# Performance work log

Hardware: AMD Instinct MI355X
Metric: run time of the kernel (lower is better)

Reference implementation:

```python
import jax, jax.numpy as jnp
import numpy as np

IMAGE_SIZE = 512
STRIDES = (8, 16, 32)
W_SEG, W_DET, W_CLS = 1.0, 1.0, 0.5


def _bce_logits(x, y):
    # numerically stable binary cross entropy with logits (broadcasts y)
    return jnp.maximum(x, 0.0) - x * y + jnp.log1p(jnp.exp(-jnp.abs(x)))


def _focal_loss_mean(logits, targets, num_classes, alpha=0.25, gamma=2.0):
    # sigmoid focal loss; targets are class indices, -1 (or any negative) => all-background row
    t = jax.nn.one_hot(targets, num_classes, dtype=logits.dtype)
    p = jax.nn.sigmoid(logits)
    ce = _bce_logits(logits, t)
    p_t = p * t + (1.0 - p) * (1.0 - t)
    a_t = alpha * t + (1.0 - alpha) * (1.0 - t)
    return jnp.mean(a_t * (1.0 - p_t) ** gamma * ce)


def _det_scale_loss(cls_logits, reg_preds, cent_preds, boxes, labels, stride):
    B, Cp1, H, W = cls_logits.shape
    C = Cp1 - 1
    L = H * W
    cls = jnp.transpose(cls_logits, (0, 2, 3, 1))[..., 1:].reshape(B, L, C)
    reg = jnp.transpose(reg_preds, (0, 2, 3, 1)).reshape(B, L, 4)
    cent = cent_preds.reshape(B, L)
    xs = (jnp.arange(W, dtype=jnp.float32) + 0.5) * stride
    ys = (jnp.arange(H, dtype=jnp.float32) + 0.5) * stride
    gy, gx = jnp.meshgrid(ys, xs, indexing='ij')
    loc_x = gx.reshape(-1)
    loc_y = gy.reshape(-1)

    def per_image(cls_i, reg_i, cent_i, gb, gl):
        b = gb * IMAGE_SIZE  # [cx,cy,w,h] in pixels
        x0 = b[:, 0] - b[:, 2] * 0.5
        y0 = b[:, 1] - b[:, 3] * 0.5
        x1 = b[:, 0] + b[:, 2] * 0.5
        y1 = b[:, 1] + b[:, 3] * 0.5
        l = loc_x[:, None] - x0[None, :]
        t = loc_y[:, None] - y0[None, :]
        r = x1[None, :] - loc_x[:, None]
        btm = y1[None, :] - loc_y[:, None]
        ltrb = jnp.stack([l, t, r, btm], axis=-1)  # (L, N, 4)
        inside = jnp.min(ltrb, axis=-1) > 0
        area = (x1 - x0) * (y1 - y0)
        masked_area = jnp.where(inside, area[None, :], jnp.inf)
        idx = jnp.argmin(masked_area, axis=-1)  # min-area matched box per location
        pos = jnp.any(inside, axis=-1)
        cls_t = jnp.where(pos, gl[idx], -1)
        reg_t = jnp.take_along_axis(ltrb, idx[:, None, None], axis=1)[:, 0, :] / stride
        lr = reg_t[:, jnp.array([0, 2])]
        tb = reg_t[:, jnp.array([1, 3])]
        eps = 1e-6
        cen_t = jnp.sqrt(jnp.clip((jnp.min(lr, -1) / (jnp.max(lr, -1) + eps)) * (jnp.min(tb, -1) / (jnp.max(tb, -1) + eps)), 0.0, 1.0))
        cls_l = _focal_loss_mean(cls_i, cls_t, C)
        npos = jnp.sum(pos)
        d = reg_i - reg_t
        sl1 = jnp.mean(jnp.where(jnp.abs(d) < 1.0, 0.5 * d * d, jnp.abs(d) - 0.5), axis=-1)
        posf = pos.astype(jnp.float32)
        denom = jnp.maximum(npos, 1).astype(jnp.float32)
        reg_l = jnp.where(npos > 0, jnp.sum(sl1 * posf) / denom, 0.0)
        bce = _bce_logits(cent_i, cen_t)
        cen_l = jnp.where(npos > 0, jnp.sum(bce * posf) / denom, 0.0)
        return cls_l, reg_l, cen_l

    cl, rl, cel = jax.vmap(per_image)(cls, reg, cent, boxes, labels)
    return jnp.mean(cl), jnp.mean(rl), jnp.mean(cel)


def _total_loss(seg_logits, seg_mask, cls_list, reg_list, cen_list, boxes, labels, cls_pred, cls_target):
    # segmentation: BCE-with-logits, integer mask broadcast as float target over channels
    seg_t = seg_mask.astype(jnp.float32)[:, None, :, :]  # (B,1,H,W) broadcasts vs (B,C,H,W)
    seg_loss = jnp.mean(_bce_logits(seg_logits, seg_t))
    tot_cls = 0.0
    tot_reg = 0.0
    tot_cen = 0.0
    for s in range(3):
        cl, rl, cel = _det_scale_loss(cls_list[s], reg_list[s], cen_list[s], boxes, labels, STRIDES[s])
        tot_cls = tot_cls + cl
        tot_reg = tot_reg + rl
        tot_cen = tot_cen + cel
    n = 3.0
    det_loss = tot_cls / n + tot_reg / n + tot_cen / n
    cls_loss = _focal_loss_mean(cls_pred, cls_target, cls_pred.shape[-1])
    return W_SEG * seg_loss + W_DET * det_loss + W_CLS * cls_loss


def setup_inputs() -> dict:
    key = jax.random.key(0)
    ks = jax.random.split(key, 16)
    B = 32
    inp = {
        'seg_logits': jax.random.normal(ks[0], (B, 4, 512, 512), jnp.float32),
        'seg_mask': jax.random.randint(ks[1], (B, 512, 512), 0, 4, jnp.int32),
        'cls_logits_s0': jax.random.normal(ks[2], (B, 5, 64, 64), jnp.float32),
        'cls_logits_s1': jax.random.normal(ks[3], (B, 5, 32, 32), jnp.float32),
        'cls_logits_s2': jax.random.normal(ks[4], (B, 5, 16, 16), jnp.float32),
        'reg_preds_s0': jax.random.normal(ks[5], (B, 4, 64, 64), jnp.float32),
        'reg_preds_s1': jax.random.normal(ks[6], (B, 4, 32, 32), jnp.float32),
        'reg_preds_s2': jax.random.normal(ks[7], (B, 4, 16, 16), jnp.float32),
        'centerness_s0': jax.random.normal(ks[8], (B, 1, 64, 64), jnp.float32),
        'centerness_s1': jax.random.normal(ks[9], (B, 1, 32, 32), jnp.float32),
        'centerness_s2': jax.random.normal(ks[10], (B, 1, 16, 16), jnp.float32),
        'boxes': jax.random.uniform(ks[11], (B, 20, 4), jnp.float32),
        'labels': jax.random.randint(ks[12], (B, 20), 0, 4, jnp.int32),
        'cls_pred': jax.random.normal(ks[13], (B, 10), jnp.float32),
        'cls_target': jax.random.randint(ks[14], (B,), 0, 10, jnp.int32),
    }
    return inp


def reference(seg_logits, seg_mask, cls_logits_s0, cls_logits_s1, cls_logits_s2, reg_preds_s0, reg_preds_s1, reg_preds_s2, centerness_s0, centerness_s1, centerness_s2, boxes, labels, cls_pred, cls_target):
    return _total_loss(seg_logits, seg_mask,
                       (cls_logits_s0, cls_logits_s1, cls_logits_s2),
                       (reg_preds_s0, reg_preds_s1, reg_preds_s2),
                       (centerness_s0, centerness_s1, centerness_s2),
                       boxes, labels, cls_pred, cls_target)
```

## Files before the change

### kernel.cpp

```cpp
#include <hip/hip_runtime.h>
#include <math.h>

#define NB 32
#define DET_BLOCKS 96
#define SEG_BLOCKS 1024
#define CHUNKS 8
#define TOTAL_BLOCKS (DET_BLOCKS + SEG_BLOCKS)


__device__ __forceinline__ float bce_logits(float x, float y) {
    float a = fabsf(x);
    return fmaxf(x, 0.f) - x * y + __logf(1.f + __expf(-a));
}

__device__ __forceinline__ float focal_elt(float x, float t) {
    float p = 1.f / (1.f + __expf(-x));
    float ce = bce_logits(x, t);
    float p_t = (t > 0.5f) ? p : (1.f - p);
    float a_t = (t > 0.5f) ? 0.25f : 0.75f;
    float om = 1.f - p_t;
    return a_t * om * om * ce;
}

template <int N>
__device__ void blk_reduce_arr(float* v) {
    __shared__ float sm[N][4];
    int lane = threadIdx.x & 63;
    int wid  = threadIdx.x >> 6;
#pragma unroll
    for (int j = 0; j < N; j++) {
        float x = v[j];
#pragma unroll
        for (int off = 32; off > 0; off >>= 1) x += __shfl_down(x, off, 64);
        if (lane == 0) sm[j][wid] = x;
    }
    __syncthreads();
    if (threadIdx.x == 0) {
#pragma unroll
        for (int j = 0; j < N; j++) {
            float s = 0.f;
#pragma unroll
            for (int w = 0; w < 4; w++) s += sm[j][w];
            v[j] = s;
        }
    }
}


__global__ __launch_bounds__(256) void fused_kernel(
        const float* __restrict__ seg_logits, const int* __restrict__ mask,
        const float* __restrict__ cls0, const float* __restrict__ cls1, const float* __restrict__ cls2,
        const float* __restrict__ reg0, const float* __restrict__ reg1, const float* __restrict__ reg2,
        const float* __restrict__ cen0, const float* __restrict__ cen1, const float* __restrict__ cen2,
        const float* __restrict__ boxes, const int* __restrict__ labels,
        float* __restrict__ segpart, float* __restrict__ detc) {

    if (blockIdx.x < DET_BLOCKS) {
        const int s = blockIdx.x >> 5;
        const int b = blockIdx.x & 31;
        int Wd, shift, L; float stride;
        const float *cls, *reg, *cen;
        if (s == 0)      { Wd = 64; shift = 6; L = 4096; stride = 8.f;  cls = cls0; reg = reg0; cen = cen0; }
        else if (s == 1) { Wd = 32; shift = 5; L = 1024; stride = 16.f; cls = cls1; reg = reg1; cen = cen1; }
        else             { Wd = 16; shift = 4; L = 256;  stride = 32.f; cls = cls2; reg = reg2; cen = cen2; }

        __shared__ float sx0[20], sy0[20], sx1[20], sy1[20], sar[20];
        __shared__ int   slb[20];
        if (threadIdx.x < 20) {
            int k = threadIdx.x;
            const float* bb = boxes + (b * 20 + k) * 4;
            float cx = bb[0] * 512.f, cy = bb[1] * 512.f;
            float w  = bb[2] * 512.f, h  = bb[3] * 512.f;
            float x0 = cx - 0.5f * w, y0 = cy - 0.5f * h;
            float x1 = cx + 0.5f * w, y1 = cy + 0.5f * h;
            sx0[k] = x0; sy0[k] = y0; sx1[k] = x1; sy1[k] = y1;
            sar[k] = (x1 - x0) * (y1 - y0);
            slb[k] = labels[b * 20 + k];
        }
        __syncthreads();

        const float* clsb = cls + (size_t)b * 5 * L;
        const float* regb = reg + (size_t)b * 4 * L;
        const float* cenb = cen + (size_t)b * L;
        const float inv = 1.f / stride;

        float cls_s = 0.f, reg_s = 0.f, cen_s = 0.f, np = 0.f;
        for (int l = threadIdx.x; l < L; l += 256) {
            float lx = ((l & (Wd - 1)) + 0.5f) * stride;
            float ly = ((l >> shift)   + 0.5f) * stride;
            int bk = -1; float ba = INFINITY;
            float bl = 0.f, btp = 0.f, brr = 0.f, bbt = 0.f;
#pragma unroll
            for (int k = 0; k < 20; k++) {
                float li = lx - sx0[k], ti = ly - sy0[k];
                float ri = sx1[k] - lx, bi = sy1[k] - ly;
                float mn = fminf(fminf(li, ti), fminf(ri, bi));
                if (mn > 0.f && sar[k] < ba) {
                    ba = sar[k]; bk = k;
                    bl = li; btp = ti; brr = ri; bbt = bi;
                }
            }
            int tl = (bk >= 0) ? slb[bk] : -1;
#pragma unroll
            for (int c = 0; c < 4; c++) {
                float x = clsb[(c + 1) * L + l];
                cls_s += focal_elt(x, (c == tl) ? 1.f : 0.f);
            }
            if (bk >= 0) {
                float r0 = bl * inv, r1 = btp * inv, r2 = brr * inv, r3 = bbt * inv;
                float d0 = regb[0 * L + l] - r0;
                float d1 = regb[1 * L + l] - r1;
                float d2 = regb[2 * L + l] - r2;
                float d3 = regb[3 * L + l] - r3;
                float a0 = fabsf(d0), a1 = fabsf(d1), a2 = fabsf(d2), a3 = fabsf(d3);
                float sl = (a0 < 1.f ? 0.5f * d0 * d0 : a0 - 0.5f)
                         + (a1 < 1.f ? 0.5f * d1 * d1 : a1 - 0.5f)
                         + (a2 < 1.f ? 0.5f * d2 * d2 : a2 - 0.5f)
                         + (a3 < 1.f ? 0.5f * d3 * d3 : a3 - 0.5f);
                reg_s += 0.25f * sl;
                float mnlr = fminf(r0, r2), mxlr = fmaxf(r0, r2);
                float mntb = fminf(r1, r3), mxtb = fmaxf(r1, r3);
                float v = (mnlr / (mxlr + 1e-6f)) * (mntb / (mxtb + 1e-6f));
                v = fminf(fmaxf(v, 0.f), 1.f);
                float ct = sqrtf(v);
                cen_s += bce_logits(cenb[l], ct);
                np += 1.f;
            }
        }

        float v4[4] = {cls_s, reg_s, cen_s, np};
        blk_reduce_arr<4>(v4);
        if (threadIdx.x == 0) {
            float cls_l = v4[0] / (L * 4.f);
            float npos  = v4[3];
            float denom = fmaxf(npos, 1.f);
            float reg_l = (npos > 0.f) ? v4[1] / denom : 0.f;
            float cen_l = (npos > 0.f) ? v4[2] / denom : 0.f;
            detc[blockIdx.x] = (cls_l + reg_l + cen_l) * (1.f / (float)DET_BLOCKS);
        }
        return;
    }

    const int HW  = 512 * 512;
    const int QPI = HW / 4;
    const int sblk = blockIdx.x - DET_BLOCKS;
    const size_t qbase = (size_t)sblk * 2048;
    const int b  = (int)(qbase >> 16);
    const int qs = (int)(qbase & 65535);
    const int t  = threadIdx.x;

    const int4*   mq = (const int4*)(mask + (size_t)b * HW) + qs;
    const float4* xq = (const float4*)(seg_logits + (size_t)b * 4 * HW) + qs;

    float acc = 0.f;
#pragma unroll 2
    for (int j = 0; j < CHUNKS; j++) {
        const int idx = j * 256 + t;
        const int4   m  = mq[idx];
        const float4 x0 = xq[0 * QPI + idx];
        const float4 x1 = xq[1 * QPI + idx];
        const float4 x2 = xq[2 * QPI + idx];
        const float4 x3 = xq[3 * QPI + idx];
        const float t0 = (float)m.x, t1 = (float)m.y, t2 = (float)m.z, t3 = (float)m.w;
        acc += bce_logits(x0.x, t0) + bce_logits(x0.y, t1)
             + bce_logits(x0.z, t2) + bce_logits(x0.w, t3);
        acc += bce_logits(x1.x, t0) + bce_logits(x1.y, t1)
             + bce_logits(x1.z, t2) + bce_logits(x1.w, t3);
        acc += bce_logits(x2.x, t0) + bce_logits(x2.y, t1)
             + bce_logits(x2.z, t2) + bce_logits(x2.w, t3);
        acc += bce_logits(x3.x, t0) + bce_logits(x3.y, t1)
             + bce_logits(x3.z, t2) + bce_logits(x3.w, t3);
    }

    float v[1] = {acc};
    blk_reduce_arr<1>(v);
    if (threadIdx.x == 0) segpart[sblk] = v[0];
}


__global__ __launch_bounds__(256) void final_kernel(
        const float* __restrict__ segpart, const float* __restrict__ detc,
        const float* __restrict__ cls_pred, const int* __restrict__ cls_target,
        float* __restrict__ out) {
    const float seg_scale = 1.f / 33554432.f;
    const float cls_scale = 0.5f / 320.f;
    float acc = 0.f;
    for (int i = threadIdx.x; i < SEG_BLOCKS; i += 256) acc += segpart[i] * seg_scale;
    if (threadIdx.x < DET_BLOCKS) acc += detc[threadIdx.x];
    for (int e = threadIdx.x; e < NB * 10; e += 256) {
        int i = e / 10, c = e - i * 10;
        acc += cls_scale * focal_elt(cls_pred[e], (cls_target[i] == c) ? 1.f : 0.f);
    }
    float v[1] = {acc};
    blk_reduce_arr<1>(v);
    if (threadIdx.x == 0) out[0] = v[0];
}


extern "C" void kernel_launch(void* const* d_in, const int* in_sizes, int n_in,
                              void* d_out, int out_size, void* d_ws, size_t ws_size,
                              hipStream_t stream) {
    const float* seg_logits = (const float*)d_in[0];
    const int*   seg_mask   = (const int*)d_in[1];
    const float* cls0 = (const float*)d_in[2];
    const float* cls1 = (const float*)d_in[3];
    const float* cls2 = (const float*)d_in[4];
    const float* reg0 = (const float*)d_in[5];
    const float* reg1 = (const float*)d_in[6];
    const float* reg2 = (const float*)d_in[7];
    const float* cen0 = (const float*)d_in[8];
    const float* cen1 = (const float*)d_in[9];
    const float* cen2 = (const float*)d_in[10];
    const float* boxes  = (const float*)d_in[11];
    const int*   labels = (const int*)d_in[12];
    const float* cls_pred   = (const float*)d_in[13];
    const int*   cls_target = (const int*)d_in[14];

    float* ws      = (float*)d_ws;
    float* segpart = ws;
    float* detc    = ws + SEG_BLOCKS;

    fused_kernel<<<TOTAL_BLOCKS, 256, 0, stream>>>(seg_logits, seg_mask,
                                                   cls0, cls1, cls2,
                                                   reg0, reg1, reg2,
                                                   cen0, cen1, cen2,
                                                   boxes, labels, segpart, detc);
    final_kernel<<<1, 256, 0, stream>>>(segpart, detc, cls_pred, cls_target,
                                        (float*)d_out);
}
```

Before: 252.8 us.

## Fuse final reduction via last-block atomic counter and double seg block count

Removes the separate final reduction kernel launch by having each block increment a global atomic counter, with the last-arriving block computing the final sum and the classification focal loss. Seg blocks are doubled to 2048, each handling half the work, with all loads issued up front into registers for more memory-level parallelism. The counter uses a modulo so it works across repeated launches without a reset, and it adds a fence and an atomic per block.

```diff
diff --git a/kernel.cpp b/kernel.cpp
--- a/kernel.cpp
+++ b/kernel.cpp
@@ -3,9 +3,10 @@
 
 #define NB 32
 #define DET_BLOCKS 96
-#define SEG_BLOCKS 1024
-#define CHUNKS 8
+#define SEG_BLOCKS 2048
 #define TOTAL_BLOCKS (DET_BLOCKS + SEG_BLOCKS)
+
+__device__ unsigned int g_done = 0u;
 
 
 __device__ __forceinline__ float bce_logits(float x, float y) {
@@ -53,7 +54,11 @@
         const float* __restrict__ reg0, const float* __restrict__ reg1, const float* __restrict__ reg2,
         const float* __restrict__ cen0, const float* __restrict__ cen1, const float* __restrict__ cen2,
         const float* __restrict__ boxes, const int* __restrict__ labels,
-        float* __restrict__ segpart, float* __restrict__ detc) {
+        const float* __restrict__ cls_pred, const int* __restrict__ cls_target,
+        float* __restrict__ segpart, float* __restrict__ detc,
+        float* __restrict__ out) {
+
+    __shared__ int last_flag;
 
     if (blockIdx.x < DET_BLOCKS) {
         const int s = blockIdx.x >> 5;
@@ -138,62 +143,71 @@
             float cen_l = (npos > 0.f) ? v4[2] / denom : 0.f;
             detc[blockIdx.x] = (cls_l + reg_l + cen_l) * (1.f / (float)DET_BLOCKS);
         }
-        return;
-    }
-
-    const int HW  = 512 * 512;
-    const int QPI = HW / 4;
-    const int sblk = blockIdx.x - DET_BLOCKS;
-    const size_t qbase = (size_t)sblk * 2048;
-    const int b  = (int)(qbase >> 16);
-    const int qs = (int)(qbase & 65535);
-    const int t  = threadIdx.x;
-
-    const int4*   mq = (const int4*)(mask + (size_t)b * HW) + qs;
-    const float4* xq = (const float4*)(seg_logits + (size_t)b * 4 * HW) + qs;
-
-    float acc = 0.f;
-#pragma unroll 2
-    for (int j = 0; j < CHUNKS; j++) {
-        const int idx = j * 256 + t;
-        const int4   m  = mq[idx];
-        const float4 x0 = xq[0 * QPI + idx];
-        const float4 x1 = xq[1 * QPI + idx];
-        const float4 x2 = xq[2 * QPI + idx];
-        const float4 x3 = xq[3 * QPI + idx];
-        const float t0 = (float)m.x, t1 = (float)m.y, t2 = (float)m.z, t3 = (float)m.w;
-        acc += bce_logits(x0.x, t0) + bce_logits(x0.y, t1)
-             + bce_logits(x0.z, t2) + bce_logits(x0.w, t3);
-        acc += bce_logits(x1.x, t0) + bce_logits(x1.y, t1)
-             + bce_logits(x1.z, t2) + bce_logits(x1.w, t3);
-        acc += bce_logits(x2.x, t0) + bce_logits(x2.y, t1)
-             + bce_logits(x2.z, t2) + bce_logits(x2.w, t3);
-        acc += bce_logits(x3.x, t0) + bce_logits(x3.y, t1)
-             + bce_logits(x3.z, t2) + bce_logits(x3.w, t3);
-    }
-
-    float v[1] = {acc};
-    blk_reduce_arr<1>(v);
-    if (threadIdx.x == 0) segpart[sblk] = v[0];
-}
-
-
-__global__ __launch_bounds__(256) void final_kernel(
-        const float* __restrict__ segpart, const float* __restrict__ detc,
-        const float* __restrict__ cls_pred, const int* __restrict__ cls_target,
-        float* __restrict__ out) {
-    const float seg_scale = 1.f / 33554432.f;
-    const float cls_scale = 0.5f / 320.f;
-    float acc = 0.f;
-    for (int i = threadIdx.x; i < SEG_BLOCKS; i += 256) acc += segpart[i] * seg_scale;
-    if (threadIdx.x < DET_BLOCKS) acc += detc[threadIdx.x];
-    for (int e = threadIdx.x; e < NB * 10; e += 256) {
-        int i = e / 10, c = e - i * 10;
-        acc += cls_scale * focal_elt(cls_pred[e], (cls_target[i] == c) ? 1.f : 0.f);
-    }
-    float v[1] = {acc};
-    blk_reduce_arr<1>(v);
-    if (threadIdx.x == 0) out[0] = v[0];
+    } else {
+        const int HW  = 512 * 512;
+        const int QPI = HW / 4;
+        const int sblk = blockIdx.x - DET_BLOCKS;
+        const size_t qbase = (size_t)sblk * 1024;
+        const int b  = (int)(qbase >> 16);
+        const int qs = (int)(qbase & 65535);
+        const int t  = threadIdx.x;
+
+        const int4*   mq = (const int4*)(mask + (size_t)b * HW) + qs;
+        const float4* xq = (const float4*)(seg_logits + (size_t)b * 4 * HW) + qs;
+
+        int4   m[4];
+        float4 a0[4], a1[4], a2[4], a3[4];
+#pragma unroll
+        for (int j = 0; j < 4; j++) {
+            const int idx = j * 256 + t;
+            m[j]  = mq[idx];
+            a0[j] = xq[0 * QPI + idx];
+            a1[j] = xq[1 * QPI + idx];
+            a2[j] = xq[2 * QPI + idx];
+            a3[j] = xq[3 * QPI + idx];
+        }
+        float acc = 0.f;
+#pragma unroll
+        for (int j = 0; j < 4; j++) {
+            const float t0 = (float)m[j].x, t1 = (float)m[j].y;
+            const float t2 = (float)m[j].z, t3 = (float)m[j].w;
+            acc += bce_logits(a0[j].x, t0) + bce_logits(a0[j].y, t1)
+                 + bce_logits(a0[j].z, t2) + bce_logits(a0[j].w, t3);
+            acc += bce_logits(a1[j].x, t0) + bce_logits(a1[j].y, t1)
+                 + bce_logits(a1[j].z, t2) + bce_logits(a1[j].w, t3);
+            acc += bce_logits(a2[j].x, t0) + bce_logits(a2[j].y, t1)
+                 + bce_logits(a2[j].z, t2) + bce_logits(a2[j].w, t3);
+            acc += bce_logits(a3[j].x, t0) + bce_logits(a3[j].y, t1)
+                 + bce_logits(a3[j].z, t2) + bce_logits(a3[j].w, t3);
+        }
+
+        float v[1] = {acc};
+        blk_reduce_arr<1>(v);
+        if (threadIdx.x == 0) segpart[sblk] = v[0];
+    }
+
+    if (threadIdx.x == 0) {
+        __threadfence();
+        unsigned old = atomicAdd(&g_done, 1u);
+        last_flag = ((old + 1u) % (unsigned)TOTAL_BLOCKS == 0u) ? 1 : 0;
+    }
+    __syncthreads();
+
+    if (last_flag) {
+        __threadfence();
+        const float seg_scale = 1.f / 33554432.f;
+        const float cls_scale = 0.5f / 320.f;
+        float acc = 0.f;
+        for (int i = threadIdx.x; i < SEG_BLOCKS; i += 256) acc += segpart[i] * seg_scale;
+        if (threadIdx.x < DET_BLOCKS) acc += detc[threadIdx.x];
+        for (int e = threadIdx.x; e < NB * 10; e += 256) {
+            int i = e / 10, c = e - i * 10;
+            acc += cls_scale * focal_elt(cls_pred[e], (cls_target[i] == c) ? 1.f : 0.f);
+        }
+        float v[1] = {acc};
+        blk_reduce_arr<1>(v);
+        if (threadIdx.x == 0) out[0] = v[0];
+    }
 }
 
 
@@ -224,7 +238,8 @@
                                                    cls0, cls1, cls2,
                                                    reg0, reg1, reg2,
                                                    cen0, cen1, cen2,
-                                                   boxes, labels, segpart, detc);
-    final_kernel<<<1, 256, 0, stream>>>(segpart, detc, cls_pred, cls_target,
-                                        (float*)d_out);
-}
+                                                   boxes, labels,
+                                                   cls_pred, cls_target,
+                                                   segpart, detc,
+                                                   (float*)d_out);
+}
```

Result: slower. 346.5 us (+37.1%).

## Split seg loss into per-plane blocks with contiguous logits and more blocks

Applied to the files above, without the earlier changes.

Reorganizes the segmentation BCE work so each block covers a contiguous 16K-float slice of a single channel plane, instead of one spatial tile read across all four channels. The number of seg blocks doubles and each block issues eight independent 16-byte loads per iteration. The mask is now reloaded once per channel rather than shared across the four channels, which adds mask traffic (likely served from cache) in exchange for more parallelism and contiguous streaming. The final kernel's fixed SEG_BLOCKS loop picks up the new count automatically.

```diff
diff --git a/kernel.cpp b/kernel.cpp
--- a/kernel.cpp
+++ b/kernel.cpp
@@ -3,14 +3,21 @@
 
 #define NB 32
 #define DET_BLOCKS 96
-#define SEG_BLOCKS 1024
-#define CHUNKS 8
+#define SEG_BLOCKS 2048
 #define TOTAL_BLOCKS (DET_BLOCKS + SEG_BLOCKS)
+
+typedef float floatx4 __attribute__((ext_vector_type(4)));
+typedef int   intx4   __attribute__((ext_vector_type(4)));
 
 
 __device__ __forceinline__ float bce_logits(float x, float y) {
     float a = fabsf(x);
     return fmaxf(x, 0.f) - x * y + __logf(1.f + __expf(-a));
+}
+
+__device__ __forceinline__ float bce4(floatx4 x, intx4 m) {
+    return bce_logits(x.x, (float)m.x) + bce_logits(x.y, (float)m.y)
+         + bce_logits(x.z, (float)m.z) + bce_logits(x.w, (float)m.w);
 }
 
 __device__ __forceinline__ float focal_elt(float x, float t) {
@@ -141,40 +148,36 @@
         return;
     }
 
-    const int HW  = 512 * 512;
-    const int QPI = HW / 4;
-    const int sblk = blockIdx.x - DET_BLOCKS;
-    const size_t qbase = (size_t)sblk * 2048;
-    const int b  = (int)(qbase >> 16);
-    const int qs = (int)(qbase & 65535);
-    const int t  = threadIdx.x;
-
-    const int4*   mq = (const int4*)(mask + (size_t)b * HW) + qs;
-    const float4* xq = (const float4*)(seg_logits + (size_t)b * 4 * HW) + qs;
+    const int s     = blockIdx.x - DET_BLOCKS;
+    const int plane = s >> 4;
+    const int b     = plane >> 2;
+    const int poff  = (s & 15) << 12;
+
+    const floatx4* Lq = (const floatx4*)seg_logits + (size_t)s * 4096;
+    const intx4*   Mq = (const intx4*)mask + (size_t)b * 65536 + poff;
+    const int t = threadIdx.x;
 
     float acc = 0.f;
 #pragma unroll 2
-    for (int j = 0; j < CHUNKS; j++) {
-        const int idx = j * 256 + t;
-        const int4   m  = mq[idx];
-        const float4 x0 = xq[0 * QPI + idx];
-        const float4 x1 = xq[1 * QPI + idx];
-        const float4 x2 = xq[2 * QPI + idx];
-        const float4 x3 = xq[3 * QPI + idx];
-        const float t0 = (float)m.x, t1 = (float)m.y, t2 = (float)m.z, t3 = (float)m.w;
-        acc += bce_logits(x0.x, t0) + bce_logits(x0.y, t1)
-             + bce_logits(x0.z, t2) + bce_logits(x0.w, t3);
-        acc += bce_logits(x1.x, t0) + bce_logits(x1.y, t1)
-             + bce_logits(x1.z, t2) + bce_logits(x1.w, t3);
-        acc += bce_logits(x2.x, t0) + bce_logits(x2.y, t1)
-             + bce_logits(x2.z, t2) + bce_logits(x2.w, t3);
-        acc += bce_logits(x3.x, t0) + bce_logits(x3.y, t1)
-             + bce_logits(x3.z, t2) + bce_logits(x3.w, t3);
+    for (int g = 0; g < 4; g++) {
+        const int base = (g << 10) + t;
+        const floatx4 x0 = Lq[base];
+        const floatx4 x1 = Lq[base + 256];
+        const floatx4 x2 = Lq[base + 512];
+        const floatx4 x3 = Lq[base + 768];
+        const intx4   m0 = Mq[base];
+        const intx4   m1 = Mq[base + 256];
+        const intx4   m2 = Mq[base + 512];
+        const intx4   m3 = Mq[base + 768];
+        acc += bce4(x0, m0);
+        acc += bce4(x1, m1);
+        acc += bce4(x2, m2);
+        acc += bce4(x3, m3);
     }
 
     float v[1] = {acc};
     blk_reduce_arr<1>(v);
-    if (threadIdx.x == 0) segpart[sblk] = v[0];
+    if (threadIdx.x == 0) segpart[s] = v[0];
 }
 
 
```

Result: faster. 247.6 us (-2.1%).
